# Optimization experiments

Hardware: AMD Instinct MI355X
Metric: run time of the kernel (lower is better)

## Reference

```python
import jax, jax.numpy as jnp
import numpy as np

B, L, H = 4, 4096, 1024
NH, W, SHIFT, FF = 16, 64, 32, 4096
HD = H // NH
EPS = 1e-5


def _ln(x, g, b):
    mu = jnp.mean(x, axis=-1, keepdims=True)
    var = jnp.var(x, axis=-1, keepdims=True)
    return (x - mu) * jax.lax.rsqrt(var + EPS) * g + b


def setup_inputs() -> dict:
    key = jax.random.key(0)
    ks = jax.random.split(key, 8)
    s = 0.02
    return {
        "x": jax.random.normal(ks[0], (B, L, H), dtype=jnp.float32),
        "ln1_g": jnp.ones((H,), jnp.float32),
        "ln1_b": jnp.zeros((H,), jnp.float32),
        "in_proj_w": jax.random.normal(ks[1], (3 * H, H), jnp.float32) * s,
        "in_proj_b": jnp.zeros((3 * H,), jnp.float32),
        "out_proj_w": jax.random.normal(ks[2], (H, H), jnp.float32) * s,
        "out_proj_b": jnp.zeros((H,), jnp.float32),
        "ln2_g": jnp.ones((H,), jnp.float32),
        "ln2_b": jnp.zeros((H,), jnp.float32),
        "w1": jax.random.normal(ks[3], (FF, H), jnp.float32) * s,
        "b1": jnp.zeros((FF,), jnp.float32),
        "w2": jax.random.normal(ks[4], (H, FF), jnp.float32) * s,
        "b2": jnp.zeros((H,), jnp.float32),
    }


def reference(x, ln1_g, ln1_b, in_proj_w, in_proj_b, out_proj_w, out_proj_b,
              ln2_g, ln2_b, w1, b1, w2, b2):
    # shift (torch.roll with negative shift)
    xs = jnp.roll(x, -SHIFT, axis=1)
    q_in = _ln(xs, ln1_g, ln1_b)
    # packed qkv projection (torch MHA in_proj)
    qkv = q_in @ in_proj_w.T + in_proj_b              # [B, L, 3H]
    q, k, v = jnp.split(qkv, 3, axis=-1)
    nW = L // W
    # block-diagonal mask == independent windows: [B, nW, W, NH, HD]
    def to_win(t):
        return t.reshape(B, nW, W, NH, HD)
    qw, kw, vw = to_win(q), to_win(k), to_win(v)
    scale = 1.0 / jnp.sqrt(jnp.float32(HD))
    scores = jnp.einsum('bnqhd,bnkhd->bnhqk', qw, kw) * scale
    attn = jax.nn.softmax(scores, axis=-1)
    o = jnp.einsum('bnhqk,bnkhd->bnqhd', attn, vw).reshape(B, L, H)
    o = o @ out_proj_w.T + out_proj_b
    xs = xs + o
    x = jnp.roll(xs, SHIFT, axis=1)  # un-shift
    z = _ln(x, ln2_g, ln2_b)
    z = jax.nn.gelu(z @ w1.T + b1, approximate=False) @ w2.T + b2
    return x + z
```

## Files before the change

### kernel.cpp

```cpp
#include <hip/hip_runtime.h>
#include <cstdint>
#include <cstddef>

#define B_ 4
#define L_ 4096
#define H_ 1024
#define NH_ 16
#define W_ 64
#define SHIFT_ 32
#define FF_ 4096
#define HD_ 64
#define MCA_ 8192
#define MCF_ 8192

typedef unsigned short u16;
typedef __attribute__((ext_vector_type(8))) __bf16 bf16x8;
typedef __attribute__((ext_vector_type(4))) float f32x4;
typedef __attribute__((ext_vector_type(4))) unsigned short u16x4;

__device__ __forceinline__ float bf2f(u16 u) {
    unsigned int x = ((unsigned int)u) << 16;
    float f;
    __builtin_memcpy(&f, &x, 4);
    return f;
}
__device__ __forceinline__ u16 f2bf(float f) {
    unsigned int u;
    __builtin_memcpy(&u, &f, 4);
    u = (u + 0x7fffu + ((u >> 16) & 1u)) >> 16;
    return (u16)u;
}

__device__ __forceinline__ void gload16(const u16* g, u16* l) {
    __builtin_amdgcn_global_load_lds(
        (const __attribute__((address_space(1))) void*)g,
        (__attribute__((address_space(3))) void*)l, 16, 0, 0);
}

__device__ __forceinline__ bf16x8 ldfrag(const u16* p) {
    uint4 v = *(const uint4*)p;
    bf16x8 r;
    __builtin_memcpy(&r, &v, 16);
    return r;
}

__device__ __forceinline__ f32x4 mfma16(bf16x8 a, bf16x8 b, f32x4 c) {
    return __builtin_amdgcn_mfma_f32_16x16x32_bf16(a, b, c, 0, 0, 0);
}

__global__ __launch_bounds__(256) void cvt_kernel(
    const float* __restrict__ src, u16* __restrict__ dst, int n4) {
    const int i = blockIdx.x * 256 + threadIdx.x;
    if (i < n4) {
        const float4 v = ((const float4*)src)[i];
        u16x4 o;
        o[0] = f2bf(v.x); o[1] = f2bf(v.y);
        o[2] = f2bf(v.z); o[3] = f2bf(v.w);
        ((u16x4*)dst)[i] = o;
    }
}

template <int GELU, int BIAS>
__global__ __launch_bounds__(256, 2) void gemm_bt(
    const u16* __restrict__ A, const u16* __restrict__ Bm, int ldb,
    const float* __restrict__ bias, u16* __restrict__ C,
    int M, int N, int K) {
    __shared__ __align__(16) u16 lA[128 * 32];
    __shared__ __align__(16) u16 lB[128 * 32];

    const int t = threadIdx.x;
    const int lane = t & 63;
    const int wv = t >> 6;
    const int wrow = wv >> 1, wcol = wv & 1;
    const int ln15 = lane & 15, quad = lane >> 4;
    const int mBase = blockIdx.y * 128;
    const int nBase = blockIdx.x * 128;

    f32x4 acc[4][4] = {};

    const int r0 = t >> 2, kc = (t & 3) * 8;
    const u16* gA0 = A + (size_t)(mBase + r0) * K + kc;
    const u16* gA1 = A + (size_t)(mBase + 64 + r0) * K + kc;
    const u16* gB0 = Bm + (size_t)(nBase + r0) * ldb + kc;
    const u16* gB1 = Bm + (size_t)(nBase + 64 + r0) * ldb + kc;
    u16* lA0 = &lA[t * 8];
    u16* lA1 = &lA[(t + 256) * 8];
    u16* lB0 = &lB[t * 8];
    u16* lB1 = &lB[(t + 256) * 8];

    for (int kt = 0; kt < K; kt += 32) {
        gload16(gA0, lA0);
        gload16(gA1, lA1);
        gload16(gB0, lB0);
        gload16(gB1, lB1);
        gA0 += 32; gA1 += 32; gB0 += 32; gB1 += 32;
        __syncthreads();

        bf16x8 aF[4], bF[4];
#pragma unroll
        for (int i = 0; i < 4; ++i)
            aF[i] = ldfrag(&lA[(wrow * 64 + i * 16 + ln15) * 32 + quad * 8]);
#pragma unroll
        for (int j = 0; j < 4; ++j)
            bF[j] = ldfrag(&lB[(wcol * 64 + j * 16 + ln15) * 32 + quad * 8]);
#pragma unroll
        for (int i = 0; i < 4; ++i)
#pragma unroll
            for (int j = 0; j < 4; ++j)
                acc[i][j] = mfma16(aF[i], bF[j], acc[i][j]);
        __syncthreads();
    }

#pragma unroll
    for (int j = 0; j < 4; ++j) {
        const int col = nBase + wcol * 64 + j * 16 + ln15;
        const float bcol = BIAS ? bias[col] : 0.0f;
#pragma unroll
        for (int i = 0; i < 4; ++i) {
#pragma unroll
            for (int r = 0; r < 4; ++r) {
                const int row = mBase + wrow * 64 + i * 16 + quad * 4 + r;
                float v = acc[i][j][r] + bcol;
                if (GELU) v = 0.5f * v * (1.0f + erff(v * 0.70710678118f));
                C[(size_t)row * N + col] = f2bf(v);
            }
        }
    }
}

__global__ __launch_bounds__(256, 4) void add_kernel(
    const u16* __restrict__ ff, const float* __restrict__ b2,
    float* __restrict__ out, int rowBase) {
    const int r = blockIdx.x;
    const size_t gOff = (size_t)(rowBase + r) * 1024;
    const int t = threadIdx.x;
    const float4 xv = ((const float4*)(out + gOff))[t];
    const u16x4 fv = ((const u16x4*)(ff + (size_t)r * 1024))[t];
    const float4 bv = ((const float4*)b2)[t];
    float4 o;
    o.x = xv.x + bf2f(fv[0]) + bv.x;
    o.y = xv.y + bf2f(fv[1]) + bv.y;
    o.z = xv.z + bf2f(fv[2]) + bv.z;
    o.w = xv.w + bf2f(fv[3]) + bv.w;
    ((float4*)(out + gOff))[t] = o;
}

__global__ __launch_bounds__(256, 4) void ln1_kernel(
    const float* __restrict__ x, const float* __restrict__ g,
    const float* __restrict__ bb, u16* __restrict__ y, int rowBase) {
    const int row = rowBase + blockIdx.x;
    const int bi = row >> 12, l = row & 4095;
    const float* src = x + ((size_t)(bi << 12) + ((l + SHIFT_) & 4095)) * 1024;
    const int t = threadIdx.x;
    const int lane = t & 63, wv = t >> 6;

    const float4 u = ((const float4*)src)[t];
    float v[4] = {u.x, u.y, u.z, u.w};
    float sum = 0.f, sq = 0.f;
#pragma unroll
    for (int k = 0; k < 4; ++k) { sum += v[k]; sq += v[k] * v[k]; }
    for (int off = 32; off > 0; off >>= 1) {
        sum += __shfl_down(sum, off);
        sq += __shfl_down(sq, off);
    }
    __shared__ float red[8];
    __shared__ float smu, srs;
    if (lane == 0) { red[wv] = sum; red[4 + wv] = sq; }
    __syncthreads();
    if (t == 0) {
        float s = red[0] + red[1] + red[2] + red[3];
        float q = red[4] + red[5] + red[6] + red[7];
        float mu = s * (1.0f / 1024.0f);
        float var = q * (1.0f / 1024.0f) - mu * mu;
        smu = mu;
        srs = rsqrtf(var + 1e-5f);
    }
    __syncthreads();
    const float mu = smu, rs = srs;
    const float4 gv = ((const float4*)g)[t];
    const float4 bv = ((const float4*)bb)[t];
    u16x4 outv;
    outv[0] = f2bf((v[0] - mu) * rs * gv.x + bv.x);
    outv[1] = f2bf((v[1] - mu) * rs * gv.y + bv.y);
    outv[2] = f2bf((v[2] - mu) * rs * gv.z + bv.z);
    outv[3] = f2bf((v[3] - mu) * rs * gv.w + bv.w);
    ((u16x4*)(y + (size_t)blockIdx.x * 1024))[t] = outv;
}

__global__ __launch_bounds__(256, 4) void ln2_kernel(
    const float* __restrict__ x, const u16* __restrict__ o2,
    const float* __restrict__ g, const float* __restrict__ bb,
    float* __restrict__ x2, u16* __restrict__ z) {
    const int row = blockIdx.x;
    const int bi = row >> 12, l = row & 4095;
    const size_t srcO = (size_t)(bi << 12) + ((l - SHIFT_) & 4095);
    const int t = threadIdx.x;
    const int lane = t & 63, wv = t >> 6;

    const float4 ux = ((const float4*)(x + (size_t)row * 1024))[t];
    const u16x4 uo = ((const u16x4*)(o2 + srcO * 1024))[t];
    float v[4];
    v[0] = ux.x + bf2f(uo[0]);
    v[1] = ux.y + bf2f(uo[1]);
    v[2] = ux.z + bf2f(uo[2]);
    v[3] = ux.w + bf2f(uo[3]);
    float sum = 0.f, sq = 0.f;
#pragma unroll
    for (int k = 0; k < 4; ++k) { sum += v[k]; sq += v[k] * v[k]; }
    float4 x2v = {v[0], v[1], v[2], v[3]};
    ((float4*)(x2 + (size_t)row * 1024))[t] = x2v;

    for (int off = 32; off > 0; off >>= 1) {
        sum += __shfl_down(sum, off);
        sq += __shfl_down(sq, off);
    }
    __shared__ float red[8];
    __shared__ float smu, srs;
    if (lane == 0) { red[wv] = sum; red[4 + wv] = sq; }
    __syncthreads();
    if (t == 0) {
        float s = red[0] + red[1] + red[2] + red[3];
        float q = red[4] + red[5] + red[6] + red[7];
        float mu = s * (1.0f / 1024.0f);
        float var = q * (1.0f / 1024.0f) - mu * mu;
        smu = mu;
        srs = rsqrtf(var + 1e-5f);
    }
    __syncthreads();
    const float mu = smu, rs = srs;
    const float4 gv = ((const float4*)g)[t];
    const float4 bv = ((const float4*)bb)[t];
    u16x4 outv;
    outv[0] = f2bf((v[0] - mu) * rs * gv.x + bv.x);
    outv[1] = f2bf((v[1] - mu) * rs * gv.y + bv.y);
    outv[2] = f2bf((v[2] - mu) * rs * gv.z + bv.z);
    outv[3] = f2bf((v[3] - mu) * rs * gv.w + bv.w);
    ((u16x4*)(z + (size_t)row * 1024))[t] = outv;
}

__global__ __launch_bounds__(256, 2) void attn_kernel(
    const u16* __restrict__ qkv, u16* __restrict__ o) {
    __shared__ __align__(16) u16 sQ[64 * 64];
    __shared__ __align__(16) u16 sK[64 * 64];
    __shared__ __align__(16) u16 sV[64 * 64];
    __shared__ float sS[64 * 66];

    const int t = threadIdx.x;
    const int win = blockIdx.x >> 4;
    const int head = blockIdx.x & 15;
    const size_t rowbase = (size_t)win * 64;
    const u16* base = qkv + rowbase * 3072 + head * 64;

    {
        const int c0 = t, c1 = t + 256;
        const int r0 = c0 >> 3, d0 = (c0 & 7) * 8;
        const int r1 = c1 >> 3, d1 = (c1 & 7) * 8;
        const u16* g0 = base + (size_t)r0 * 3072 + d0;
        const u16* g1 = base + (size_t)r1 * 3072 + d1;
        gload16(g0, &sQ[c0 * 8]);
        gload16(g1, &sQ[c1 * 8]);
        gload16(g0 + 1024, &sK[c0 * 8]);
        gload16(g1 + 1024, &sK[c1 * 8]);
        gload16(g0 + 2048, &sV[c0 * 8]);
        gload16(g1 + 2048, &sV[c1 * 8]);
    }
    __syncthreads();

    const int lane = t & 63, wv = t >> 6;
    const int ln15 = lane & 15, quad = lane >> 4;

    f32x4 accS[4] = {};
#pragma unroll
    for (int kb = 0; kb < 2; ++kb) {
        bf16x8 aF = ldfrag(&sQ[(wv * 16 + ln15) * 64 + kb * 32 + quad * 8]);
#pragma unroll
        for (int jt = 0; jt < 4; ++jt) {
            bf16x8 bF = ldfrag(&sK[(jt * 16 + ln15) * 64 + kb * 32 + quad * 8]);
            accS[jt] = mfma16(aF, bF, accS[jt]);
        }
    }
#pragma unroll
    for (int jt = 0; jt < 4; ++jt)
#pragma unroll
        for (int r = 0; r < 4; ++r)
            sS[(wv * 16 + quad * 4 + r) * 66 + jt * 16 + ln15] =
                accS[jt][r] * 0.125f;
    __syncthreads();

    {
        const int row = t >> 2, part = t & 3;
        const float* sr = &sS[row * 66 + part * 16];
        float vals[16];
        float mx = -1e30f;
#pragma unroll
        for (int i = 0; i < 16; ++i) {
            vals[i] = sr[i];
            mx = fmaxf(mx, vals[i]);
        }
        mx = fmaxf(mx, __shfl_xor(mx, 1));
        mx = fmaxf(mx, __shfl_xor(mx, 2));
        float sum = 0.f;
#pragma unroll
        for (int i = 0; i < 16; ++i) {
            vals[i] = __expf(vals[i] - mx);
            sum += vals[i];
        }
        sum += __shfl_xor(sum, 1);
        sum += __shfl_xor(sum, 2);
        const float inv = 1.0f / sum;
        u16* pr = &sQ[row * 64 + part * 16];
#pragma unroll
        for (int i = 0; i < 16; ++i) pr[i] = f2bf(vals[i] * inv);
    }
    __syncthreads();

    f32x4 accO[4] = {};
#pragma unroll
    for (int kb = 0; kb < 2; ++kb) {
        bf16x8 aF = ldfrag(&sQ[(wv * 16 + ln15) * 64 + kb * 32 + quad * 8]);
#pragma unroll
        for (int dt = 0; dt < 4; ++dt) {
            u16 tmp[8];
#pragma unroll
            for (int j = 0; j < 8; ++j)
                tmp[j] = sV[(kb * 32 + quad * 8 + j) * 64 + dt * 16 + ln15];
            bf16x8 bF;
            __builtin_memcpy(&bF, tmp, 16);
            accO[dt] = mfma16(aF, bF, accO[dt]);
        }
    }
    u16* ob = o + rowbase * 1024 + head * 64;
#pragma unroll
    for (int dt = 0; dt < 4; ++dt)
#pragma unroll
        for (int r = 0; r < 4; ++r) {
            const int q = wv * 16 + quad * 4 + r;
            const int d = dt * 16 + ln15;
            ob[(size_t)q * 1024 + d] = f2bf(accO[dt][r]);
        }
}

extern "C" void kernel_launch(void* const* d_in, const int* in_sizes, int n_in,
                              void* d_out, int out_size, void* d_ws,
                              size_t ws_size, hipStream_t stream) {
    (void)in_sizes; (void)n_in; (void)out_size; (void)ws_size;
    const float* x = (const float*)d_in[0];
    const float* ln1_g = (const float*)d_in[1];
    const float* ln1_b = (const float*)d_in[2];
    const float* in_proj_w = (const float*)d_in[3];
    const float* in_proj_b = (const float*)d_in[4];
    const float* out_proj_w = (const float*)d_in[5];
    const float* out_proj_b = (const float*)d_in[6];
    const float* ln2_g = (const float*)d_in[7];
    const float* ln2_b = (const float*)d_in[8];
    const float* w1 = (const float*)d_in[9];
    const float* b1 = (const float*)d_in[10];
    const float* w2 = (const float*)d_in[11];
    const float* b2 = (const float*)d_in[12];
    float* out = (float*)d_out;

    char* ws = (char*)d_ws;
    const size_t MB = 1024 * 1024;
    u16* wb_w1 = (u16*)(ws + 0 * MB);
    u16* wb_w2 = (u16*)(ws + 8 * MB);
    u16* wb_inproj = (u16*)(ws + 16 * MB);
    u16* wb_outproj = (u16*)(ws + 22 * MB);
    u16* qkv_c = (u16*)(ws + 24 * MB);
    u16* o2 = (u16*)(ws + 72 * MB);
    u16* z = (u16*)(ws + 16 * MB);
    u16* h_buf = (u16*)(ws + 48 * MB);
    u16* ff_c = (u16*)(ws + 112 * MB);

    u16* qin = (u16*)d_out;
    u16* o_full = (u16*)((char*)d_out + 16 * MB);
    float* x2 = out;

    const int M = B_ * L_;

    cvt_kernel<<<(FF_ * H_ / 4 + 255) / 256, 256, 0, stream>>>(
        w1, wb_w1, FF_ * H_ / 4);
    cvt_kernel<<<(H_ * FF_ / 4 + 255) / 256, 256, 0, stream>>>(
        w2, wb_w2, H_ * FF_ / 4);
    cvt_kernel<<<(3 * H_ * H_ / 4 + 255) / 256, 256, 0, stream>>>(
        in_proj_w, wb_inproj, 3 * H_ * H_ / 4);
    cvt_kernel<<<(H_ * H_ / 4 + 255) / 256, 256, 0, stream>>>(
        out_proj_w, wb_outproj, H_ * H_ / 4);

    for (int c = 0; c < 2; ++c) {
        const int rowBase = c * MCA_;
        ln1_kernel<<<MCA_, 256, 0, stream>>>(x, ln1_g, ln1_b, qin, rowBase);
        gemm_bt<0, 1><<<dim3(3 * H_ / 128, MCA_ / 128), 256, 0, stream>>>(
            qin, wb_inproj, H_, in_proj_b, qkv_c, MCA_, 3 * H_, H_);
        attn_kernel<<<(MCA_ / W_) * NH_, 256, 0, stream>>>(
            qkv_c, o_full + (size_t)rowBase * H_);
    }
    gemm_bt<0, 1><<<dim3(H_ / 128, M / 128), 256, 0, stream>>>(
        o_full, wb_outproj, H_, out_proj_b, o2, M, H_, H_);

    ln2_kernel<<<M, 256, 0, stream>>>(x, o2, ln2_g, ln2_b, x2, z);

    for (int c = 0; c < 2; ++c) {
        const int rowBase = c * MCF_;
        const size_t off = (size_t)rowBase * H_;
        gemm_bt<1, 1><<<dim3(FF_ / 128, MCF_ / 128), 256, 0, stream>>>(
            z + off, wb_w1, H_, b1, h_buf, MCF_, FF_, H_);
        gemm_bt<0, 0><<<dim3(H_ / 128, MCF_ / 128), 256, 0, stream>>>(
            h_buf, wb_w2, FF_, nullptr, ff_c, MCF_, H_, FF_);
        add_kernel<<<MCF_, 256, 0, stream>>>(ff_c, b2, out, rowBase);
    }
}
```

Baseline: 838.1 us.

## Replace GEMM with 256x256-tile multi-buffered swizzled kernel and split FFN along FF

Replaces the 128x128 single-buffered GEMM with a 512-thread 256x256 tile kernel. It keeps four LDS stages with XOR-swizzled layout, issues async prefetch three steps ahead, and raises wave priority around the MFMA blocks. The FFN is restructured to split the hidden dimension into two 2048-wide halves over all rows. The second GEMM accumulates in fp32 directly into the output, which removes the bf16 intermediate and the separate add kernel. The trade-offs are more LDS per block, fewer resident blocks, and a read-modify-write of the output in the epilogue.

After: 908.4 us. 8.4% more time.

```diff
diff --git a/kernel.cpp b/kernel.cpp
--- a/kernel.cpp
+++ b/kernel.cpp
@@ -11,7 +11,6 @@
 #define FF_ 4096
 #define HD_ 64
 #define MCA_ 8192
-#define MCF_ 8192
 
 typedef unsigned short u16;
 typedef __attribute__((ext_vector_type(8))) __bf16 bf16x8;
@@ -60,89 +59,124 @@
     }
 }
 
-template <int GELU, int BIAS>
-__global__ __launch_bounds__(256, 2) void gemm_bt(
-    const u16* __restrict__ A, const u16* __restrict__ Bm, int ldb,
-    const float* __restrict__ bias, u16* __restrict__ C,
-    int M, int N, int K) {
-    __shared__ __align__(16) u16 lA[128 * 32];
-    __shared__ __align__(16) u16 lB[128 * 32];
-
-    const int t = threadIdx.x;
-    const int lane = t & 63;
-    const int wv = t >> 6;
-    const int wrow = wv >> 1, wcol = wv & 1;
-    const int ln15 = lane & 15, quad = lane >> 4;
-    const int mBase = blockIdx.y * 128;
-    const int nBase = blockIdx.x * 128;
-
-    f32x4 acc[4][4] = {};
-
-    const int r0 = t >> 2, kc = (t & 3) * 8;
-    const u16* gA0 = A + (size_t)(mBase + r0) * K + kc;
-    const u16* gA1 = A + (size_t)(mBase + 64 + r0) * K + kc;
-    const u16* gB0 = Bm + (size_t)(nBase + r0) * ldb + kc;
-    const u16* gB1 = Bm + (size_t)(nBase + 64 + r0) * ldb + kc;
-    u16* lA0 = &lA[t * 8];
-    u16* lA1 = &lA[(t + 256) * 8];
-    u16* lB0 = &lB[t * 8];
-    u16* lB1 = &lB[(t + 256) * 8];
-
-    for (int kt = 0; kt < K; kt += 32) {
-        gload16(gA0, lA0);
-        gload16(gA1, lA1);
-        gload16(gB0, lB0);
-        gload16(gB1, lB1);
-        gA0 += 32; gA1 += 32; gB0 += 32; gB1 += 32;
-        __syncthreads();
-
-        bf16x8 aF[4], bF[4];
-#pragma unroll
-        for (int i = 0; i < 4; ++i)
-            aF[i] = ldfrag(&lA[(wrow * 64 + i * 16 + ln15) * 32 + quad * 8]);
-#pragma unroll
-        for (int j = 0; j < 4; ++j)
-            bF[j] = ldfrag(&lB[(wcol * 64 + j * 16 + ln15) * 32 + quad * 8]);
+template <int GELU, int BIAS, int F32OUT>
+__global__ __launch_bounds__(512, 2) void gemm256(
+    const u16* __restrict__ A, const u16* __restrict__ Bm,
+    int lda, int ldb, const float* __restrict__ bias,
+    void* __restrict__ Cv, int N, int K) {
+    __shared__ __align__(16) u16 lds[4 * 16384];
+
+    const int tid = threadIdx.x;
+    const int lane = tid & 63;
+    const int wv = tid >> 6;
+    const int wr = wv >> 2;
+    const int wc = wv & 3;
+    const int ln15 = lane & 15;
+    const int quad = lane >> 4;
+    const int mBase = blockIdx.y * 256;
+    const int nBase = blockIdx.x * 256;
+    const int nt = K >> 5;
+
+    const int sr = tid >> 3;
+    const int src = (tid & 7) ^ (sr & 7);
+    const int grow = sr * 2 + (src >> 2);
+    const int gk = (src & 3) * 8;
+    const u16* gA = A + (size_t)(mBase + grow) * lda + gk;
+    const u16* gB = Bm + (size_t)(nBase + grow) * ldb + gk;
+    u16* dstA = &lds[tid * 8];
+    u16* dstB = &lds[8192 + tid * 8];
+
+    const int sw = ((ln15 & 1) * 4 + quad) ^ (ln15 >> 1);
+    const int offA = (wr * 64 + (ln15 >> 1)) * 64 + sw * 8;
+    const int offB = (wc * 32 + (ln15 >> 1)) * 64 + sw * 8;
+
+    f32x4 acc[8][4] = {};
+
+#pragma unroll
+    for (int p = 0; p < 3; ++p) {
+        const u16* a = gA + p * 32;
+        const u16* b = gB + p * 32;
+        u16* la = dstA + p * 16384;
+        u16* lb = dstB + p * 16384;
+        gload16(a, la);
+        gload16(a + (size_t)128 * lda, la + 4096);
+        gload16(b, lb);
+        gload16(b + (size_t)128 * ldb, lb + 4096);
+    }
+    asm volatile("s_waitcnt vmcnt(8)" ::: "memory");
+    __builtin_amdgcn_s_barrier();
+    __builtin_amdgcn_sched_barrier(0);
+
+    for (int tt = 0; tt < nt; ++tt) {
+        const u16* lA = &lds[(tt & 3) * 16384];
+        const u16* lB = lA + 8192;
+        bf16x8 aF[4], bF[4], aG[4];
+#pragma unroll
+        for (int i = 0; i < 4; ++i) aF[i] = ldfrag(lA + offA + i * 512);
+#pragma unroll
+        for (int j = 0; j < 4; ++j) bF[j] = ldfrag(lB + offB + j * 512);
+        if (tt + 3 < nt) {
+            const u16* a = gA + (size_t)(tt + 3) * 32;
+            u16* la = dstA + ((tt + 3) & 3) * 16384;
+            gload16(a, la);
+            gload16(a + (size_t)128 * lda, la + 4096);
+        }
+        __builtin_amdgcn_s_barrier();
+        __builtin_amdgcn_s_setprio(1);
 #pragma unroll
         for (int i = 0; i < 4; ++i)
 #pragma unroll
             for (int j = 0; j < 4; ++j)
                 acc[i][j] = mfma16(aF[i], bF[j], acc[i][j]);
-        __syncthreads();
-    }
-
-#pragma unroll
-    for (int j = 0; j < 4; ++j) {
-        const int col = nBase + wcol * 64 + j * 16 + ln15;
+        __builtin_amdgcn_s_setprio(0);
+#pragma unroll
+        for (int i = 0; i < 4; ++i) aG[i] = ldfrag(lA + offA + (i + 4) * 512);
+        if (tt + 3 < nt) {
+            const u16* b = gB + (size_t)(tt + 3) * 32;
+            u16* lb = dstB + ((tt + 3) & 3) * 16384;
+            gload16(b, lb);
+            gload16(b + (size_t)128 * ldb, lb + 4096);
+        }
+        __builtin_amdgcn_s_barrier();
+        __builtin_amdgcn_s_setprio(1);
+#pragma unroll
+        for (int i = 0; i < 4; ++i)
+#pragma unroll
+            for (int j = 0; j < 4; ++j)
+                acc[i + 4][j] = mfma16(aG[i], bF[j], acc[i + 4][j]);
+        __builtin_amdgcn_s_setprio(0);
+        if (tt < nt - 1) {
+            if (tt <= nt - 4)
+                asm volatile("s_waitcnt vmcnt(8)" ::: "memory");
+            else if (tt == nt - 3)
+                asm volatile("s_waitcnt vmcnt(4)" ::: "memory");
+            else
+                asm volatile("s_waitcnt vmcnt(0)" ::: "memory");
+            __builtin_amdgcn_s_barrier();
+            __builtin_amdgcn_sched_barrier(0);
+        }
+    }
+
+    const int r0 = mBase + wr * 128 + quad * 4;
+    const int c0 = nBase + wc * 64 + ln15;
+#pragma unroll
+    for (int fn = 0; fn < 4; ++fn) {
+        const int col = c0 + fn * 16;
         const float bcol = BIAS ? bias[col] : 0.0f;
 #pragma unroll
-        for (int i = 0; i < 4; ++i) {
+        for (int fm = 0; fm < 8; ++fm) {
 #pragma unroll
             for (int r = 0; r < 4; ++r) {
-                const int row = mBase + wrow * 64 + i * 16 + quad * 4 + r;
-                float v = acc[i][j][r] + bcol;
+                const int row = r0 + fm * 16 + r;
+                float v = acc[fm][fn][r] + bcol;
                 if (GELU) v = 0.5f * v * (1.0f + erff(v * 0.70710678118f));
-                C[(size_t)row * N + col] = f2bf(v);
+                if (F32OUT)
+                    ((float*)Cv)[(size_t)row * N + col] += v;
+                else
+                    ((u16*)Cv)[(size_t)row * N + col] = f2bf(v);
             }
         }
     }
-}
-
-__global__ __launch_bounds__(256, 4) void add_kernel(
-    const u16* __restrict__ ff, const float* __restrict__ b2,
-    float* __restrict__ out, int rowBase) {
-    const int r = blockIdx.x;
-    const size_t gOff = (size_t)(rowBase + r) * 1024;
-    const int t = threadIdx.x;
-    const float4 xv = ((const float4*)(out + gOff))[t];
-    const u16x4 fv = ((const u16x4*)(ff + (size_t)r * 1024))[t];
-    const float4 bv = ((const float4*)b2)[t];
-    float4 o;
-    o.x = xv.x + bf2f(fv[0]) + bv.x;
-    o.y = xv.y + bf2f(fv[1]) + bv.y;
-    o.z = xv.z + bf2f(fv[2]) + bv.z;
-    o.w = xv.w + bf2f(fv[3]) + bv.w;
-    ((float4*)(out + gOff))[t] = o;
 }
 
 __global__ __launch_bounds__(256, 4) void ln1_kernel(
@@ -369,7 +403,6 @@
     u16* o2 = (u16*)(ws + 72 * MB);
     u16* z = (u16*)(ws + 16 * MB);
     u16* h_buf = (u16*)(ws + 48 * MB);
-    u16* ff_c = (u16*)(ws + 112 * MB);
 
     u16* qin = (u16*)d_out;
     u16* o_full = (u16*)((char*)d_out + 16 * MB);
@@ -389,23 +422,22 @@
     for (int c = 0; c < 2; ++c) {
         const int rowBase = c * MCA_;
         ln1_kernel<<<MCA_, 256, 0, stream>>>(x, ln1_g, ln1_b, qin, rowBase);
-        gemm_bt<0, 1><<<dim3(3 * H_ / 128, MCA_ / 128), 256, 0, stream>>>(
-            qin, wb_inproj, H_, in_proj_b, qkv_c, MCA_, 3 * H_, H_);
+        gemm256<0, 1, 0><<<dim3(3 * H_ / 256, MCA_ / 256), 512, 0, stream>>>(
+            qin, wb_inproj, H_, H_, in_proj_b, qkv_c, 3 * H_, H_);
         attn_kernel<<<(MCA_ / W_) * NH_, 256, 0, stream>>>(
             qkv_c, o_full + (size_t)rowBase * H_);
     }
-    gemm_bt<0, 1><<<dim3(H_ / 128, M / 128), 256, 0, stream>>>(
-        o_full, wb_outproj, H_, out_proj_b, o2, M, H_, H_);
+    gemm256<0, 1, 0><<<dim3(H_ / 256, M / 256), 512, 0, stream>>>(
+        o_full, wb_outproj, H_, H_, out_proj_b, o2, H_, H_);
 
     ln2_kernel<<<M, 256, 0, stream>>>(x, o2, ln2_g, ln2_b, x2, z);
 
-    for (int c = 0; c < 2; ++c) {
-        const int rowBase = c * MCF_;
-        const size_t off = (size_t)rowBase * H_;
-        gemm_bt<1, 1><<<dim3(FF_ / 128, MCF_ / 128), 256, 0, stream>>>(
-            z + off, wb_w1, H_, b1, h_buf, MCF_, FF_, H_);
-        gemm_bt<0, 0><<<dim3(H_ / 128, MCF_ / 128), 256, 0, stream>>>(
-            h_buf, wb_w2, FF_, nullptr, ff_c, MCF_, H_, FF_);
-        add_kernel<<<MCF_, 256, 0, stream>>>(ff_c, b2, out, rowBase);
-    }
-}
+    gemm256<1, 1, 0><<<dim3(2048 / 256, M / 256), 512, 0, stream>>>(
+        z, wb_w1, H_, H_, b1, h_buf, 2048, H_);
+    gemm256<0, 0, 1><<<dim3(H_ / 256, M / 256), 512, 0, stream>>>(
+        h_buf, wb_w2, 2048, FF_, nullptr, out, H_, 2048);
+    gemm256<1, 1, 0><<<dim3(2048 / 256, M / 256), 512, 0, stream>>>(
+        z, wb_w1 + (size_t)2048 * H_, H_, H_, b1 + 2048, h_buf, 2048, H_);
+    gemm256<0, 1, 1><<<dim3(H_ / 256, M / 256), 512, 0, stream>>>(
+        h_buf, wb_w2 + 2048, 2048, FF_, b2, out, H_, 2048);
+}
```
